# Kernel tuning notes

Hardware: AMD Instinct MI355X
Metric: run time of the kernel (lower is better)

## Reference

```python
import jax, jax.numpy as jnp
import numpy as np

B, H, W, C = 2, 128, 128, 192
HEADS = 6
HD = C // HEADS
WS = 16
OWIN = int(WS * 0.5) + WS          # 24
PAD = (OWIN - WS) // 2             # 4
NQ = WS * WS
NK = OWIN * OWIN
EPS = 1e-6
HID = ((int(C * 2.667) + 7) // 8) * 8  # 512


def _rel_pos_index():
    cq = np.stack(np.meshgrid(np.arange(WS), np.arange(WS), indexing='ij')).reshape(2, -1)
    ck = np.stack(np.meshgrid(np.arange(OWIN), np.arange(OWIN), indexing='ij')).reshape(2, -1)
    rel = (ck[:, None, :] - cq[:, :, None]).transpose(1, 2, 0).astype(np.int64)  # (nq, nk, 2)
    rel[:, :, 0] += WS - 1
    rel[:, :, 1] += WS - 1
    rel[:, :, 0] *= WS + OWIN - 1
    return rel.sum(-1)  # (nq, nk)

RPI = jnp.asarray(_rel_pos_index())


def setup_inputs() -> dict:
    key = jax.random.key(0)
    ks = jax.random.split(key, 16)
    def w(k, shape, s=0.02):
        return jax.random.normal(k, shape, jnp.float32) * s
    return {
        'x': jax.random.normal(ks[0], (B, H * W, C), jnp.float32),
        'qkv_w': w(ks[1], (3 * C, C)), 'qkv_b': jnp.zeros((3 * C,), jnp.float32),
        'proj_w': w(ks[2], (C, C)), 'proj_b': jnp.zeros((C,), jnp.float32),
        'rpb': w(ks[3], ((WS + OWIN - 1) ** 2, HEADS)),
        'n1_w': jnp.ones((C,), jnp.float32), 'n1_b': jnp.zeros((C,), jnp.float32),
        'ls1': jnp.full((C,), 1e-6, jnp.float32),
        'n2_w': jnp.ones((C,), jnp.float32), 'n2_b': jnp.zeros((C,), jnp.float32),
        'ls2': jnp.full((C,), 1e-6, jnp.float32),
        'fcgv_w': w(ks[4], (2 * HID, C)), 'fcgv_b': jnp.zeros((2 * HID,), jnp.float32),
        'dw_w': w(ks[5], (HID, 1, 3, 3)), 'dw_b': jnp.zeros((HID,), jnp.float32),
        'dwd_w': w(ks[6], (HID, 1, 3, 3)), 'dwd_b': jnp.zeros((HID,), jnp.float32),
        'dil_scale': w(ks[7], (1,), 0.1),
        'fco_w': w(ks[8], (C, HID)), 'fco_b': jnp.zeros((C,), jnp.float32),
    }


def _iln(x, wgt, bias):
    # spatially-holistic LN: stats over (L, C); returns normed x and residual scale
    xf = x.astype(jnp.float32)
    mean = xf.mean(axis=(1, 2), keepdims=True)
    var = ((xf - mean) ** 2).mean(axis=(1, 2), keepdims=True)
    std = jnp.sqrt(var + EPS)
    scale = jnp.minimum(std, 2.0)  # std_ema buffer initialized to 1.0 (eval path)
    xn = (xf - mean) / scale
    return (xn * wgt + bias).astype(x.dtype), scale


def _oca(x, qkv_w, qkv_b, proj_w, proj_b, rpb):
    b = x.shape[0]
    nh, nw = H // WS, W // WS
    nwin = b * nh * nw
    qkv = x @ qkv_w.T + qkv_b
    q, k, v = jnp.split(qkv, 3, axis=-1)
    # non-overlapping query windows: (nwin, heads, nq, hd)
    qw = q.reshape(b, nh, WS, nw, WS, C).transpose(0, 1, 3, 2, 4, 5)
    qw = qw.reshape(nwin, NQ, HEADS, HD).transpose(0, 2, 1, 3)
    # overlapping K/V windows via unfold(kernel=OWIN, stride=WS, pad=PAD)
    kv = jnp.concatenate([k, v], axis=-1).reshape(b, H, W, 2 * C).transpose(0, 3, 1, 2)
    kvp = jnp.pad(kv, ((0, 0), (0, 0), (PAD, PAD), (PAD, PAD)))
    ih = (jnp.arange(nh) * WS)[:, None] + jnp.arange(OWIN)[None, :]
    iw = (jnp.arange(nw) * WS)[:, None] + jnp.arange(OWIN)[None, :]
    kvw = kvp[:, :, ih][:, :, :, :, iw]               # (b, 2C, nh, owin, nw, owin)
    kvw = kvw.transpose(0, 2, 4, 3, 5, 1).reshape(nwin, NK, 2 * C)
    kw = kvw[..., :C].reshape(nwin, NK, HEADS, HD).transpose(0, 2, 1, 3)
    vw = kvw[..., C:].reshape(nwin, NK, HEADS, HD).transpose(0, 2, 1, 3)
    bias = rpb[RPI].transpose(2, 0, 1)                # (heads, nq, nk)
    logits = jnp.einsum('whqd,whkd->whqk', qw, kw) * (HD ** -0.5) + bias
    attn = jax.nn.softmax(logits, axis=-1)
    out = jnp.einsum('whqk,whkd->whqd', attn, vw)
    out = out.transpose(0, 2, 1, 3).reshape(nwin, NQ, C) @ proj_w.T + proj_b
    # window reverse -> (b, H*W, C)
    out = out.reshape(b, nh, nw, WS, WS, C).transpose(0, 1, 3, 2, 4, 5).reshape(b, H * W, C)
    return out


def _dw(x, wgt, bias, dil):
    y = jax.lax.conv_general_dilated(x, wgt, (1, 1), [(dil, dil), (dil, dil)],
                                     rhs_dilation=(dil, dil), feature_group_count=HID)
    return y + bias[None, :, None, None]


def _ffn(x, fcgv_w, fcgv_b, dw_w, dw_b, dwd_w, dwd_b, dil_scale, fco_w, fco_b):
    gv = x @ fcgv_w.T + fcgv_b
    g, val = jnp.split(gv, 2, axis=-1)
    h = jax.nn.silu(g) * val
    h = h.transpose(0, 2, 1).reshape(-1, HID, H, W)
    h = _dw(h, dw_w, dw_b, 1)
    h = h + dil_scale[0] * _dw(h, dwd_w, dwd_b, 2)
    h = h.reshape(-1, HID, H * W).transpose(0, 2, 1)
    return h @ fco_w.T + fco_b


def reference(x, qkv_w, qkv_b, proj_w, proj_b, rpb, n1_w, n1_b, ls1, n2_w, n2_b, ls2,
              fcgv_w, fcgv_b, dw_w, dw_b, dwd_w, dwd_b, dil_scale, fco_w, fco_b):
    xn, std1 = _iln(x, n1_w, n1_b)
    x = x + std1 * (ls1 * _oca(xn, qkv_w, qkv_b, proj_w, proj_b, rpb))
    xn2, std2 = _iln(x, n2_w, n2_b)
    x = x + std2 * (ls2 * _ffn(xn2, fcgv_w, fcgv_b, dw_w, dw_b, dwd_w, dwd_b, dil_scale, fco_w, fco_b))
    return x
```

## Files before the change

kernel.cpp:

```cpp
#include <hip/hip_runtime.h>

#define DI __device__ __forceinline__

typedef __attribute__((ext_vector_type(8))) short bh8;
typedef __attribute__((ext_vector_type(4))) float fx4;
typedef __attribute__((ext_vector_type(16))) float fx16;

DI short f2bf(float f) {
  unsigned u = __builtin_bit_cast(unsigned, f);
  u += 0x7FFFu + ((u >> 16) & 1u);
  return (short)(u >> 16);
}
DI float bf2f(short s) {
  unsigned u = ((unsigned)(unsigned short)s) << 16;
  return __builtin_bit_cast(float, u);
}
DI fx4 mfma16(bh8 a, bh8 b, fx4 c) {
  return __builtin_amdgcn_mfma_f32_16x16x32_bf16(a, b, c, 0, 0, 0);
}
DI fx16 mfma32(bh8 a, bh8 b, fx16 c) {
  return __builtin_amdgcn_mfma_f32_32x32x16_bf16(a, b, c, 0, 0, 0);
}
DI fx4 fzero() { fx4 z = {0.f, 0.f, 0.f, 0.f}; return z; }

// ... 28 lines not shown
__global__ __launch_bounds__(256) void iln_partial(const float* __restrict__ x,
                                                   float* __restrict__ part) {
  const int blk = blockIdx.x, tid = threadIdx.x;
  const fx4* p = (const fx4*)(x + (size_t)blk * 12288);
  float s = 0.f, s2 = 0.f;
#pragma unroll
  for (int i = 0; i < 12; i++) {
    fx4 v = p[i * 256 + tid];
    s  += v[0] + v[1] + v[2] + v[3];
    s2 += v[0] * v[0] + v[1] * v[1] + v[2] * v[2] + v[3] * v[3];
  }
  __shared__ float sm[512];
  sm[tid] = s; sm[256 + tid] = s2;
  __syncthreads();
  for (int st = 128; st > 0; st >>= 1) {
    if (tid < st) { sm[tid] += sm[tid + st]; sm[256 + tid] += sm[256 + tid + st]; }
    __syncthreads();
  }
  if (tid == 0) { part[blk * 2] = sm[0]; part[blk * 2 + 1] = sm[256]; }
}

__global__ __launch_bounds__(256) void iln_final(const float* __restrict__ part,
                                                 const float* __restrict__ w,
                                                 const float* __restrict__ bias,
                                                 float* __restrict__ aff,
                                                 float* __restrict__ st) {
  const int b = blockIdx.x, tid = threadIdx.x;
  __shared__ float sm[512];
  sm[tid]       = part[(b * 256 + tid) * 2];
  sm[256 + tid] = part[(b * 256 + tid) * 2 + 1];
  __syncthreads();
  for (int s = 128; s > 0; s >>= 1) {
    if (tid < s) { sm[tid] += sm[tid + s]; sm[256 + tid] += sm[256 + tid + s]; }
    __syncthreads();
  }
  const float invn = 1.f / 3145728.f;
  float mean = sm[0] * invn;
  float var  = sm[256] * invn - mean * mean;
  float scale = fminf(sqrtf(var + 1e-6f), 2.f);
  if (tid < 192) {
    float a = w[tid] / scale;
    aff[(b * 192 + tid) * 2]     = a;
    aff[(b * 192 + tid) * 2 + 1] = bias[tid] - mean * a;
  }
  if (tid == 0) { st[b * 2] = mean; st[b * 2 + 1] = scale; }
}

__global__ __launch_bounds__(256) void cvt_w(const float* __restrict__ qkv_w,
                                             const float* __restrict__ proj_w,
                                             const float* __restrict__ fcgv_w,
                                             const float* __restrict__ fco_w,
                                             short* __restrict__ wbuf) {
  int t = blockIdx.x * 256 + threadIdx.x;
  int off = t * 8;
  const float* src;
  if (off < 110592)       src = qkv_w + off;
  else if (off < 147456)  src = proj_w + (off - 110592);
  else if (off < 344064)  src = fcgv_w + (off - 147456);
  else                    src = fco_w + (off - 344064);
  *(bh8*)(wbuf + off) = pack8(src);
}

__global__ __launch_bounds__(256) void cvt_aff(const float* __restrict__ src,
                                               const float* __restrict__ aff,
                                               short* __restrict__ dst) {
  int t = blockIdx.x * 256 + threadIdx.x;
  int row = t / 24;
  int c0 = (t - row * 24) * 8;
  const float* affp = aff + (row >> 14) * 384 + c0 * 2;
  *(bh8*)(dst + (size_t)t * 8) = pack8_aff(src + (size_t)row * 192 + c0, affp);
}

__global__ __launch_bounds__(256) void bias_gen(const float* __restrict__ rpb,
                                                float* __restrict__ btf) {
  int t = blockIdx.x * 256 + threadIdx.x;
  int lane = t & 63;
  int u = t >> 6;
  int qi = u & 1; int u2 = u >> 1;
  int ki = u2 & 1; u2 >>= 1;
  int kc = u2 % 9; u2 = u2 / 9;
  int w = u2 & 3, head = u2 >> 2;
  int c = lane & 31, hi = lane >> 5;
  int q = w * 64 + qi * 32 + c;
  int qterm = (q >> 4) * 39 + (q & 15);
  (void)ki; (void)kc;
  float o[16];
#pragma unroll
  for (int r = 0; r < 16; r++) {
    int k = (u & 0x3c) ? 0 : 0;
    (void)k;
    int kk = ((u >> 2) % 9) * 64 + ((u >> 1) & 1) * 32 + (r & 3) + 8 * (r >> 2) + 4 * hi;
    int ky = (kk * 2731) >> 16;
    int kx = kk - ky * 24;
    int idx = ky * 39 + kx + 600 - qterm;
    o[r] = rpb[idx * 6 + head] * 1.4426950408889634f;
  }
  fx4* dst = (fx4*)btf;
#pragma unroll
  for (int j = 0; j < 4; j++) {
    fx4 v = {o[4 * j], o[4 * j + 1], o[4 * j + 2], o[4 * j + 3]};
    dst[((size_t)u * 4 + j) * 64 + lane] = v;
  }
}

__global__ __launch_bounds__(256) void gemm_qkv(const short* __restrict__ xn,
                                                const short* __restrict__ wq,
                                                const float* __restrict__ wb,
                                                short* __restrict__ qb,
                                                short* __restrict__ kb,
                                                short* __restrict__ vb) {
  __shared__ short As[128 * 40];
  __shared__ short Bs[96 * 40];
  const int m0 = blockIdx.x * 128, by = blockIdx.y, n0 = by * 96;
  const int tid = threadIdx.x, wid = tid >> 6, lane = tid & 63;
  const int g = lane >> 4, h = lane & 15;
  const int wm = wid >> 1, wn = wid & 1;
  fx4 acc[4][3];
#pragma unroll
  for (int i = 0; i < 4; i++)
#pragma unroll
    for (int j = 0; j < 3; j++) acc[i][j] = fzero();

  for (int kt = 0; kt < 6; kt++) {
    const int k0 = kt * 32;
#pragma unroll
    for (int i = 0; i < 2; i++) {
      int ch = tid + i * 256;
      int row = ch >> 2, sl = ch & 3;
      *(bh8*)&As[row * 40 + sl * 8] = *(const bh8*)(xn + (size_t)(m0 + row) * 192 + k0 + sl * 8);
    }
    {
      int row = tid >> 2, sl = tid & 3;
      *(bh8*)&Bs[row * 40 + sl * 8] = *(const bh8*)(wq + (size_t)(n0 + row) * 192 + k0 + sl * 8);
      int ch = tid + 256;
      if (ch < 384) {
        row = ch >> 2; sl = ch & 3;
        *(bh8*)&Bs[row * 40 + sl * 8] = *(const bh8*)(wq + (size_t)(n0 + row) * 192 + k0 + sl * 8);
      }
    }
    __syncthreads();
    bh8 af[4];
#pragma unroll
    for (int mi = 0; mi < 4; mi++)
      af[mi] = *(bh8*)&As[(wm * 64 + mi * 16 + h) * 40 + g * 8];
#pragma unroll
    for (int ni = 0; ni < 3; ni++) {
      bh8 bf = *(bh8*)&Bs[(wn * 48 + ni * 16 + h) * 40 + g * 8];
#pragma unroll
      for (int mi = 0; mi < 4; mi++) acc[mi][ni] = mfma16(af[mi], bf, acc[mi][ni]);
    }
    __syncthreads();
  }
  const int seg = by >> 1;
  short* dst = (seg == 0) ? qb : (seg == 1 ? kb : vb);
  const float sc = (seg == 1) ? 0.25503486f : 1.0f;
  const int colbase = (by & 1) * 96;
#pragma unroll
  for (int mi = 0; mi < 4; mi++)
#pragma unroll
    for (int ni = 0; ni < 3; ni++)
#pragma unroll
      for (int r = 0; r < 4; r++) {
        int row = m0 + wm * 64 + mi * 16 + g * 4 + r;
        int col = colbase + wn * 48 + ni * 16 + h;
        dst[(size_t)row * 192 + col] = f2bf((acc[mi][ni][r] + wb[seg * 192 + col]) * sc);
      }
}

__global__ __launch_bounds__(256, 3) void attn_kernel(const short* __restrict__ qb,
                                                      const short* __restrict__ kb,
                                                      const short* __restrict__ vb,
                                                      const float* __restrict__ btf,
                                                      short* __restrict__ ao) {
  __shared__ short K_lds[2][64 * 40];
  __shared__ short Vt_lds[2][32 * 72];
  __shared__ float l_lds[256];
  const int tid = threadIdx.x;
  const int win = blockIdx.x, head = blockIdx.y;
  const int b = win >> 6, wy = (win >> 3) & 7, wx = win & 7;
  const int w = tid >> 6, lane = tid & 63, c = lane & 31, hi = lane >> 5;

  bh8 qf[2][2];
#pragma unroll
  for (int qi = 0; qi < 2; qi++) {
    int ql = w * 64 + qi * 32 + c;
    size_t gl = (size_t)(b * 16384 + (wy * 16 + (ql >> 4)) * 128 + wx * 16 + (ql & 15));
#pragma unroll
    for (int ds = 0; ds < 2; ds++)
      qf[qi][ds] = *(const bh8*)(qb + gl * 192 + head * 32 + ds * 16 + hi * 8);
  }
  float l_run[2] = {0.f, 0.f};
  fx16 out[2];
#pragma unroll
  for (int r = 0; r < 16; r++) { out[0][r] = 0.f; out[1][r] = 0.f; }

  const fx4* btf4 = (const fx4*)btf;
  const int hw9 = (head * 4 + w) * 9;

  const int kl_a = tid >> 2, part_a = tid & 3;
  const int kl_b = tid & 63, hg_b = tid >> 6;

  auto load_kv = [&](int kc, bh8& kr, bh8& vr) {
    int key = kc * 64 + kl_a;
    int ky = key / 24, kx = key - ky * 24;
    int py = wy * 16 - 4 + ky, px = wx * 16 - 4 + kx;
    bh8 kv = {};
    if ((unsigned)py < 128u && (unsigned)px < 128u)
      kv = *(const bh8*)(kb + ((size_t)(b * 16384 + py * 128 + px)) * 192 + head * 32 + part_a * 8);
    kr = kv;
    int key2 = kc * 64 + kl_b;
    int ky2 = key2 / 24, kx2 = key2 - ky2 * 24;
    int py2 = wy * 16 - 4 + ky2, px2 = wx * 16 - 4 + kx2;
    bh8 vv = {};
    if ((unsigned)py2 < 128u && (unsigned)px2 < 128u)
      vv = *(const bh8*)(vb + ((size_t)(b * 16384 + py2 * 128 + px2)) * 192 + head * 32 + hg_b * 8);
    vr = vv;
  };

  {
    bh8 k0r, v0r;
    load_kv(0, k0r, v0r);
    *(bh8*)&K_lds[0][kl_a * 40 + part_a * 8] = k0r;
#pragma unroll
    for (int j = 0; j < 8; j++) Vt_lds[0][(hg_b * 8 + j) * 72 + kl_b] = v0r[j];
  }
  int cur = 0;

  for (int kc = 0; kc < 9; kc++) {
    bh8 kn, vn;
    if (kc < 8) load_kv(kc + 1, kn, vn);
    __syncthreads();

    const fx4* base_kc = btf4 + (size_t)(hw9 + kc) * 1024 + lane;
#pragma unroll
    for (int ki = 0; ki < 2; ki++) {
      fx16 st[2];
#pragma unroll
      for (int qi = 0; qi < 2; qi++) {
        const fx4* bp = base_kc + (ki * 2 + qi) * 256;
        fx4 b0 = bp[0], b1 = bp[64], b2 = bp[128], b3 = bp[192];
#pragma unroll
        for (int m = 0; m < 4; m++) {
          st[qi][m]      = b0[m];
          st[qi][4 + m]  = b1[m];
          st[qi][8 + m]  = b2[m];
          st[qi][12 + m] = b3[m];
        }
      }
#pragma unroll
      for (int ds = 0; ds < 2; ds++) {
        bh8 kf = *(bh8*)&K_lds[cur][(ki * 32 + c) * 40 + ds * 16 + hi * 8];
        st[0] = mfma32(kf, qf[0][ds], st[0]);
        st[1] = mfma32(kf, qf[1][ds], st[1]);
      }
#pragma unroll
      for (int qi = 0; qi < 2; qi++) {
        float s = 0.f;
#pragma unroll
        for (int r = 0; r < 16; r++) {
          float p = fexp2(st[qi][r]);
          st[qi][r] = p;
          s += p;
        }
        l_run[qi] += s;
      }
      int dwq[2][2][4];
#pragma unroll
      for (int qi = 0; qi < 2; qi++)
#pragma unroll
        for (int k1 = 0; k1 < 2; k1++)
#pragma unroll
          for (int p01 = 0; p01 < 2; p01++) {
            int rA = 2 * p01 + 8 * k1;
            int A, Bv;
            asm("v_cvt_pk_bf16_f32 %0, %1, %2" : "=v"(A)  : "v"(st[qi][rA]),     "v"(st[qi][rA + 1]));
            asm("v_cvt_pk_bf16_f32 %0, %1, %2" : "=v"(Bv) : "v"(st[qi][rA + 4]), "v"(st[qi][rA + 5]));
#if __has_builtin(__builtin_amdgcn_permlane32_swap)
            auto pr = __builtin_amdgcn_permlane32_swap((unsigned)A, (unsigned)Bv, false, false);
            dwq[qi][k1][p01]     = (int)pr[0];
            dwq[qi][k1][p01 + 2] = (int)pr[1];
#else
            int Ax = __shfl_xor(A, 32);
            int Bx = __shfl_xor(Bv, 32);
            dwq[qi][k1][p01]     = hi ? Bx : A;
            dwq[qi][k1][p01 + 2] = hi ? Bv : Ax;
#endif
          }
#pragma unroll
      for (int k1 = 0; k1 < 2; k1++) {
        bh8 bv2 = *(bh8*)&Vt_lds[cur][c * 72 + (ki * 2 + k1) * 16 + hi * 8];
#pragma unroll
        for (int qi = 0; qi < 2; qi++) {
          int4 t4 = {dwq[qi][k1][0], dwq[qi][k1][1], dwq[qi][k1][2], dwq[qi][k1][3]};
          out[qi] = mfma32(__builtin_bit_cast(bh8, t4), bv2, out[qi]);
        }
      }
    }
    if (kc < 8) {
      *(bh8*)&K_lds[cur ^ 1][kl_a * 40 + part_a * 8] = kn;
#pragma unroll
      for (int j = 0; j < 8; j++) Vt_lds[cur ^ 1][(hg_b * 8 + j) * 72 + kl_b] = vn[j];
    }
    cur ^= 1;
  }
#pragma unroll
  for (int qi = 0; qi < 2; qi++) {
    float lp = l_run[qi] + __shfl_xor(l_run[qi], 32);
    l_lds[w * 64 + qi * 32 + c] = 1.f / lp;
  }
  __syncthreads();
#pragma unroll
  for (int qi = 0; qi < 2; qi++)
#pragma unroll
    for (int r = 0; r < 16; r++) {
      int row = (r & 3) + 8 * (r >> 2) + 4 * hi;
      float val = out[qi][r] * l_lds[w * 64 + qi * 32 + row];
      int ql = w * 64 + qi * 32 + row;
      ao[((size_t)(win * 256 + ql)) * 192 + head * 32 + c] = f2bf(val);
    }
}

__global__ __launch_bounds__(256) void gemm_proj(const short* __restrict__ ao,
                                                 const short* __restrict__ wp,
                                                 const float* __restrict__ wb,
                                                 const float* __restrict__ x,
                                                 const float* __restrict__ ls1,
                                                 const float* __restrict__ st,
                                                 float* __restrict__ x1,
                                                 float* __restrict__ part2) {
  __shared__ short As[128 * 40];
  __shared__ short Bs[96 * 40];
  const int m0 = blockIdx.x * 128, by = blockIdx.y, n0 = by * 96;
  const int tid = threadIdx.x, wid = tid >> 6, lane = tid & 63;
  const int g = lane >> 4, h = lane & 15;
  const int wm = wid >> 1, wn = wid & 1;
  fx4 acc[4][3];
#pragma unroll
  for (int i = 0; i < 4; i++)
#pragma unroll
    for (int j = 0; j < 3; j++) acc[i][j] = fzero();

  for (int kt = 0; kt < 6; kt++) {
    const int k0 = kt * 32;
#pragma unroll
    for (int i = 0; i < 2; i++) {
      int ch = tid + i * 256;
      int row = ch >> 2, sl = ch & 3;
      *(bh8*)&As[row * 40 + sl * 8] = *(const bh8*)(ao + (size_t)(m0 + row) * 192 + k0 + sl * 8);
    }
    {
      int row = tid >> 2, sl = tid & 3;
      *(bh8*)&Bs[row * 40 + sl * 8] = *(const bh8*)(wp + (size_t)(n0 + row) * 192 + k0 + sl * 8);
      int ch = tid + 256;
      if (ch < 384) {
        row = ch >> 2; sl = ch & 3;
        *(bh8*)&Bs[row * 40 + sl * 8] = *(const bh8*)(wp + (size_t)(n0 + row) * 192 + k0 + sl * 8);
      }
    }
    __syncthreads();
    bh8 af[4];
#pragma unroll
    for (int mi = 0; mi < 4; mi++)
      af[mi] = *(bh8*)&As[(wm * 64 + mi * 16 + h) * 40 + g * 8];
#pragma unroll
    for (int ni = 0; ni < 3; ni++) {
      bh8 bf = *(bh8*)&Bs[(wn * 48 + ni * 16 + h) * 40 + g * 8];
#pragma unroll
      for (int mi = 0; mi < 4; mi++) acc[mi][ni] = mfma16(af[mi], bf, acc[mi][ni]);
    }
    __syncthreads();
  }
  float ps = 0.f, ps2 = 0.f;
#pragma unroll
  for (int mi = 0; mi < 4; mi++)
#pragma unroll
    for (int ni = 0; ni < 3; ni++)
#pragma unroll
      for (int r = 0; r < 4; r++) {
        int grow = m0 + wm * 64 + mi * 16 + g * 4 + r;
        int win = grow >> 8, q = grow & 255;
        int bb = win >> 6, wy = (win >> 3) & 7, wxx = win & 7;
        int l = (wy * 16 + (q >> 4)) * 128 + wxx * 16 + (q & 15);
        int col = n0 + wn * 48 + ni * 16 + h;
        size_t di = ((size_t)(bb * 16384 + l)) * 192 + col;
        float s1 = st[bb * 2 + 1];
        float val = x[di] + s1 * ls1[col] * (acc[mi][ni][r] + wb[col]);
        x1[di] = val;
        ps += val;
        ps2 += val * val;
      }
  float* red = (float*)As;
  red[tid] = ps; red[256 + tid] = ps2;
  __syncthreads();
  for (int s = 128; s > 0; s >>= 1) {
    if (tid < s) { red[tid] += red[tid + s]; red[256 + tid] += red[256 + tid + s]; }
    __syncthreads();
  }
  if (tid == 0) {
    int pi = blockIdx.x * 2 + by;
    part2[pi * 2] = red[0];
    part2[pi * 2 + 1] = red[256];
  }
}

__global__ __launch_bounds__(256) void gemm_fcgv(const short* __restrict__ x1n,
                                                 const short* __restrict__ wg,
                                                 const float* __restrict__ wb,
                                                 short* __restrict__ hp) {
  __shared__ short smem[128 * 40 + 128 * 40];
  short* As = smem;
  short* Bs = smem + 128 * 40;
  const int m0 = blockIdx.x * 128, n0 = blockIdx.y * 64;
  const int b = m0 >> 14, l0 = m0 & 16383;
  const int tid = threadIdx.x, wid = tid >> 6, lane = tid & 63;
  const int g = lane >> 4, h = lane & 15;
  const int wm = wid >> 1, wn = wid & 1;
  fx4 accg[4][2], accv[4][2];
#pragma unroll
  for (int i = 0; i < 4; i++)
#pragma unroll
    for (int j = 0; j < 2; j++) { accg[i][j] = fzero(); accv[i][j] = fzero(); }

  for (int kt = 0; kt < 6; kt++) {
    const int k0 = kt * 32;
#pragma unroll
    for (int i = 0; i < 2; i++) {
      int ch = tid + i * 256;
      int row = ch >> 2, sl = ch & 3;
      *(bh8*)&As[row * 40 + sl * 8] = *(const bh8*)(x1n + (size_t)(m0 + row) * 192 + k0 + sl * 8);
    }
#pragma unroll
    for (int i = 0; i < 2; i++) {
      int ch = tid + i * 256;
      int row = ch >> 2, sl = ch & 3;
      int wrow = (row < 64) ? (n0 + row) : (512 + n0 + row - 64);
      *(bh8*)&Bs[row * 40 + sl * 8] = *(const bh8*)(wg + (size_t)wrow * 192 + k0 + sl * 8);
    }
    __syncthreads();
    bh8 af[4];
#pragma unroll
    for (int mi = 0; mi < 4; mi++)
      af[mi] = *(bh8*)&As[(wm * 64 + mi * 16 + h) * 40 + g * 8];
#pragma unroll
    for (int ni = 0; ni < 2; ni++) {
      bh8 bg = *(bh8*)&Bs[(wn * 32 + ni * 16 + h) * 40 + g * 8];
      bh8 bv = *(bh8*)&Bs[(64 + wn * 32 + ni * 16 + h) * 40 + g * 8];
#pragma unroll
      for (int mi = 0; mi < 4; mi++) {
        accg[mi][ni] = mfma16(af[mi], bg, accg[mi][ni]);
        accv[mi][ni] = mfma16(af[mi], bv, accv[mi][ni]);
      }
    }
    __syncthreads();
  }
  short hs[4][2][4];
#pragma unroll
  for (int mi = 0; mi < 4; mi++)
#pragma unroll
    for (int ni = 0; ni < 2; ni++)
#pragma unroll
      for (int r = 0; r < 4; r++) {
        int colg = n0 + wn * 32 + ni * 16 + h;
        float gv = accg[mi][ni][r] + wb[colg];
        float vv = accv[mi][ni][r] + wb[512 + colg];
        hs[mi][ni][r] = f2bf(gv / (1.f + __expf(-gv)) * vv);
      }
  short* T = smem;
#pragma unroll
  for (int mi = 0; mi < 4; mi++)
#pragma unroll
    for (int ni = 0; ni < 2; ni++)
#pragma unroll
      for (int r = 0; r < 4; r++) {
        int cc = wn * 32 + ni * 16 + h;
        int rl = wm * 64 + mi * 16 + g * 4 + r;
        T[cc * 136 + rl] = hs[mi][ni][r];
      }
  __syncthreads();
#pragma unroll
  for (int i = 0; i < 4; i++) {
    int ch = tid + i * 256;
    int cc = ch >> 4, lg = ch & 15;
    bh8 v = *(bh8*)&T[cc * 136 + lg * 8];
    *(bh8*)(hp + (((size_t)(b * 512 + n0 + cc)) << 14) + l0 + lg * 8) = v;
  }
}

__global__ __launch_bounds__(256, 2) void dw_fused(const short* __restrict__ in,
                                                   const float* __restrict__ w1,
                                                   const float* __restrict__ b1,
                                                   const float* __restrict__ w2,
                                                   const float* __restrict__ b2,
                                                   const float* __restrict__ dsc,
                                                   short* __restrict__ outp) {
  __shared__ short P[136 * 128];
  __shared__ short D[136 * 128];
  const int p = blockIdx.x, c = p & 511;
  const int tid = threadIdx.x;
#pragma unroll
  for (int i = 0; i < 8; i++) {
    int gs = i * 256 + tid;
    int yy = gs >> 4, sl = gs & 15;
    bh8 v = *(const bh8*)(in + ((size_t)p << 14) + gs * 8);
    *(bh8*)&P[yy * 136 + sl * 8] = v;
  }
  float k1[9], k2[9];
#pragma unroll
  for (int j = 0; j < 9; j++) { k1[j] = w1[c * 9 + j]; k2[j] = w2[c * 9 + j]; }
  const float bias1 = b1[c], bias2 = b2[c], ds = dsc[0];
  const int y = tid >> 1, hf = tid & 1;
  __syncthreads();

#pragma unroll
  for (int g = 0; g < 8; g++) {
    const int x0 = hf * 64 + g * 8;
    float acc[8];
#pragma unroll
    for (int i = 0; i < 8; i++) acc[i] = bias1;
#pragma unroll
    for (int ky = 0; ky < 3; ky++) {
// ... 19 lines not shown
  __syncthreads();

#pragma unroll
  for (int g = 0; g < 8; g++) {
    const int x0 = hf * 64 + g * 8;
    float acc[8], center[8];
#pragma unroll
    for (int i = 0; i < 8; i++) acc[i] = bias2;
#pragma unroll
    for (int ky = 0; ky < 3; ky++) {
      int yy = y + (ky - 1) * 2;
      if ((unsigned)yy < 128u) {
        const short* row = &D[yy * 136];
        float f[12];
        bh8 v = *(const bh8*)&row[x0];
#pragma unroll
        for (int j = 0; j < 8; j++) f[j + 2] = bf2f(v[j]);
        if (x0 == 0) { f[0] = 0.f; f[1] = 0.f; }
        else {
          unsigned lp = *(const unsigned*)&row[x0 - 2];
          f[0] = __builtin_bit_cast(float, lp << 16);
          f[1] = __builtin_bit_cast(float, lp & 0xffff0000u);
        }
        if (x0 == 120) { f[10] = 0.f; f[11] = 0.f; }
        else {
          unsigned rp = *(const unsigned*)&row[x0 + 8];
          f[10] = __builtin_bit_cast(float, rp << 16);
          f[11] = __builtin_bit_cast(float, rp & 0xffff0000u);
        }
        float w0 = k2[ky * 3], wA = k2[ky * 3 + 1], wB = k2[ky * 3 + 2];
#pragma unroll
        for (int i = 0; i < 8; i++) acc[i] += f[i] * w0 + f[i + 2] * wA + f[i + 4] * wB;
        if (ky == 1) {
#pragma unroll
          for (int i = 0; i < 8; i++) center[i] = f[i + 2];
        }
      }
    }
    bh8 pk;
#pragma unroll
    for (int i = 0; i < 8; i++) pk[i] = f2bf(center[i] + ds * acc[i]);
    *(bh8*)(outp + ((size_t)p << 14) + y * 128 + x0) = pk;
  }
}

__global__ __launch_bounds__(256) void gemm_fco(const short* __restrict__ h2,
                                                const short* __restrict__ wo,
                                                const float* __restrict__ wb,
                                                const float* __restrict__ x1,
                                                const float* __restrict__ ls2,
                                                const float* __restrict__ st,
                                                float* __restrict__ out) {
  __shared__ short As[128 * 40];
  __shared__ short Bs[96 * 40];
  const int m0 = blockIdx.x * 128, by = blockIdx.y, n0 = by * 96;
  const int b = m0 >> 14, l0 = m0 & 16383;
  const int tid = threadIdx.x, wid = tid >> 6, lane = tid & 63;
  const int g = lane >> 4, h = lane & 15;
  const int wm = wid >> 1, wn = wid & 1;
  const int cp = tid & 15, lg = tid >> 4;
  fx4 acc[4][3];
#pragma unroll
  for (int i = 0; i < 4; i++)
#pragma unroll
    for (int j = 0; j < 3; j++) acc[i][j] = fzero();

  for (int kt = 0; kt < 16; kt++) {
    const int k0 = kt * 32;
    {
      const short* basep = h2 + (((size_t)(b * 512 + k0 + 2 * cp)) << 14) + l0 + lg * 8;
      bh8 v0 = *(const bh8*)basep;
      bh8 v1 = *(const bh8*)(basep + 16384);
#pragma unroll
      for (int j = 0; j < 8; j++) {
        unsigned pkv = (unsigned)(unsigned short)v0[j] | (((unsigned)(unsigned short)v1[j]) << 16);
        *(unsigned*)&As[(lg * 8 + j) * 40 + 2 * cp] = pkv;
      }
    }
    {
      int row = tid >> 2, sl = tid & 3;
      *(bh8*)&Bs[row * 40 + sl * 8] = *(const bh8*)(wo + (size_t)(n0 + row) * 512 + k0 + sl * 8);
      int ch = tid + 256;
      if (ch < 384) {
        row = ch >> 2; sl = ch & 3;
        *(bh8*)&Bs[row * 40 + sl * 8] = *(const bh8*)(wo + (size_t)(n0 + row) * 512 + k0 + sl * 8);
      }
    }
    __syncthreads();
    bh8 af[4];
#pragma unroll
    for (int mi = 0; mi < 4; mi++)
      af[mi] = *(bh8*)&As[(wm * 64 + mi * 16 + h) * 40 + g * 8];
#pragma unroll
    for (int ni = 0; ni < 3; ni++) {
      bh8 bf = *(bh8*)&Bs[(wn * 48 + ni * 16 + h) * 40 + g * 8];
#pragma unroll
      for (int mi = 0; mi < 4; mi++) acc[mi][ni] = mfma16(af[mi], bf, acc[mi][ni]);
    }
    __syncthreads();
  }
  float s2 = st[b * 2 + 1];
#pragma unroll
  for (int mi = 0; mi < 4; mi++)
#pragma unroll
    for (int ni = 0; ni < 3; ni++)
#pragma unroll
      for (int r = 0; r < 4; r++) {
        int row = m0 + wm * 64 + mi * 16 + g * 4 + r;
        int col = n0 + wn * 48 + ni * 16 + h;
        size_t di = (size_t)row * 192 + col;
        out[di] = x1[di] + s2 * ls2[col] * (acc[mi][ni][r] + wb[col]);
      }
}

extern "C" void kernel_launch(void* const* d_in, const int* in_sizes, int n_in,
                              void* d_out, int out_size, void* d_ws, size_t ws_size,
                              hipStream_t stream) {
  const float* x      = (const float*)d_in[0];
  const float* qkv_w  = (const float*)d_in[1];
  const float* qkv_b  = (const float*)d_in[2];
  const float* proj_w = (const float*)d_in[3];
  const float* proj_b = (const float*)d_in[4];
  const float* rpb    = (const float*)d_in[5];
  const float* n1_w   = (const float*)d_in[6];
  const float* n1_b   = (const float*)d_in[7];
  const float* ls1    = (const float*)d_in[8];
  const float* n2_w   = (const float*)d_in[9];
  const float* n2_b   = (const float*)d_in[10];
  const float* ls2    = (const float*)d_in[11];
  const float* fcgv_w = (const float*)d_in[12];
  const float* fcgv_b = (const float*)d_in[13];
  const float* dw_w   = (const float*)d_in[14];
  const float* dw_b   = (const float*)d_in[15];
  const float* dwd_w  = (const float*)d_in[16];
  const float* dwd_b  = (const float*)d_in[17];
  const float* dil    = (const float*)d_in[18];
  const float* fco_w  = (const float*)d_in[19];
  const float* fco_b  = (const float*)d_in[20];
  float* out = (float*)d_out;
  char* ws = (char*)d_ws;

  short* wbuf = (short*)(ws + 0);
  short* wq = wbuf;
  short* wp = wbuf + 110592;
  short* wg = wbuf + 147456;
  short* wo = wbuf + 344064;
  float* part  = (float*)(ws + 884736);
  float* aff1  = (float*)(ws + 888832);
  float* aff2  = (float*)(ws + 890368);
  float* st1   = (float*)(ws + 891904);
  float* st2   = (float*)(ws + 891968);
  float* part2 = (float*)(ws + 892032);
  short* xn  = (short*)(ws + 1048576);
  float* btf = (float*)(ws + 13631488);
  short* qb  = (short*)(ws + 17301504);
  short* kb  = (short*)(ws + 29884416);
  short* vb  = (short*)(ws + 42467328);
  short* ao  = (short*)(ws + 55050240);
  float* x1  = (float*)(ws + 1048576);
  short* x1n = (short*)(ws + 26214400);
  short* hp  = (short*)(ws + 42467328);

  cvt_w<<<216, 256, 0, stream>>>(qkv_w, proj_w, fcgv_w, fco_w, wbuf);
  iln_partial<<<512, 256, 0, stream>>>(x, part);
  iln_final<<<2, 256, 0, stream>>>(part, n1_w, n1_b, aff1, st1);
  cvt_aff<<<3072, 256, 0, stream>>>(x, aff1, xn);
  bias_gen<<<216, 256, 0, stream>>>(rpb, btf);
  gemm_qkv<<<dim3(256, 6), 256, 0, stream>>>(xn, wq, qkv_b, qb, kb, vb);
  attn_kernel<<<dim3(128, 6), 256, 0, stream>>>(qb, kb, vb, btf, ao);
  gemm_proj<<<dim3(256, 2), 256, 0, stream>>>(ao, wp, proj_b, x, ls1, st1, x1, part2);
  iln_final<<<2, 256, 0, stream>>>(part2, n2_w, n2_b, aff2, st2);
  cvt_aff<<<3072, 256, 0, stream>>>(x1, aff2, x1n);
  gemm_fcgv<<<dim3(256, 8), 256, 0, stream>>>(x1n, wg, fcgv_b, hp);
  dw_fused<<<1024, 256, 0, stream>>>(hp, dw_w, dw_b, dwd_w, dwd_b, dil, hp);
  gemm_fco<<<dim3(256, 2), 256, 0, stream>>>(hp, wo, fco_b, x1, ls2, st2, out);
}
```

Before: 189.7 us.

## Split attention query rows across two blocks per window-head for more parallelism

The attention kernel now launches two blocks per (window, head), each handling 128 queries with one 32-row query tile per wave instead of two. This doubles the grid from 768 to 1536 blocks and lowers per-thread register use, raising the occupancy hint to 6 blocks per CU, so more waves are available to hide latency on a chip with many CUs. The cost is that each K/V chunk is loaded from global memory and staged into LDS twice, once per half-block. The row-sum is also rewritten as a tree reduction, and a dead statement in bias_gen is removed.

```diff
diff --git a/kernel.cpp b/kernel.cpp
--- a/kernel.cpp
+++ b/kernel.cpp
@@ -139,8 +139,6 @@
   float o[16];
 #pragma unroll
   for (int r = 0; r < 16; r++) {
-    int k = (u & 0x3c) ? 0 : 0;
-    (void)k;
     int kk = ((u >> 2) % 9) * 64 + ((u >> 1) & 1) * 32 + (r & 3) + 8 * (r >> 2) + 4 * hi;
     int ky = (kk * 2731) >> 16;
     int kx = kk - ky * 24;
@@ -219,35 +217,36 @@
       }
 }
 
-__global__ __launch_bounds__(256, 3) void attn_kernel(const short* __restrict__ qb,
+__global__ __launch_bounds__(256, 6) void attn_kernel(const short* __restrict__ qb,
                                                       const short* __restrict__ kb,
                                                       const short* __restrict__ vb,
                                                       const float* __restrict__ btf,
                                                       short* __restrict__ ao) {
   __shared__ short K_lds[2][64 * 40];
   __shared__ short Vt_lds[2][32 * 72];
-  __shared__ float l_lds[256];
+  __shared__ float l_lds[128];
   const int tid = threadIdx.x;
-  const int win = blockIdx.x, head = blockIdx.y;
+  const int win = blockIdx.x >> 1, qh = blockIdx.x & 1, head = blockIdx.y;
   const int b = win >> 6, wy = (win >> 3) & 7, wx = win & 7;
   const int w = tid >> 6, lane = tid & 63, c = lane & 31, hi = lane >> 5;
-
-  bh8 qf[2][2];
-#pragma unroll
-  for (int qi = 0; qi < 2; qi++) {
-    int ql = w * 64 + qi * 32 + c;
+  const int qblk = qh * 4 + w;
+  const int worig = qblk >> 1, qi = qblk & 1;
+
+  bh8 qf[2];
+  {
+    int ql = qblk * 32 + c;
     size_t gl = (size_t)(b * 16384 + (wy * 16 + (ql >> 4)) * 128 + wx * 16 + (ql & 15));
 #pragma unroll
     for (int ds = 0; ds < 2; ds++)
-      qf[qi][ds] = *(const bh8*)(qb + gl * 192 + head * 32 + ds * 16 + hi * 8);
-  }
-  float l_run[2] = {0.f, 0.f};
-  fx16 out[2];
-#pragma unroll
-  for (int r = 0; r < 16; r++) { out[0][r] = 0.f; out[1][r] = 0.f; }
+      qf[ds] = *(const bh8*)(qb + gl * 192 + head * 32 + ds * 16 + hi * 8);
+  }
+  float l_run = 0.f;
+  fx16 out;
+#pragma unroll
+  for (int r = 0; r < 16; r++) out[r] = 0.f;
 
   const fx4* btf4 = (const fx4*)btf;
-  const int hw9 = (head * 4 + w) * 9;
+  const int hw9 = (head * 4 + worig) * 9;
 
   const int kl_a = tid >> 2, part_a = tid & 3;
   const int kl_b = tid & 63, hg_b = tid >> 6;
@@ -283,69 +282,65 @@
     if (kc < 8) load_kv(kc + 1, kn, vn);
     __syncthreads();
 
-    const fx4* base_kc = btf4 + (size_t)(hw9 + kc) * 1024 + lane;
+    const fx4* base_kc = btf4 + (size_t)(hw9 + kc) * 1024 + qi * 256 + lane;
 #pragma unroll
     for (int ki = 0; ki < 2; ki++) {
-      fx16 st[2];
-#pragma unroll
-      for (int qi = 0; qi < 2; qi++) {
-        const fx4* bp = base_kc + (ki * 2 + qi) * 256;
+      fx16 st;
+      {
+        const fx4* bp = base_kc + ki * 512;
         fx4 b0 = bp[0], b1 = bp[64], b2 = bp[128], b3 = bp[192];
 #pragma unroll
         for (int m = 0; m < 4; m++) {
-          st[qi][m]      = b0[m];
-          st[qi][4 + m]  = b1[m];
-          st[qi][8 + m]  = b2[m];
-          st[qi][12 + m] = b3[m];
+          st[m]      = b0[m];
+          st[4 + m]  = b1[m];
+          st[8 + m]  = b2[m];
+          st[12 + m] = b3[m];
         }
       }
 #pragma unroll
       for (int ds = 0; ds < 2; ds++) {
         bh8 kf = *(bh8*)&K_lds[cur][(ki * 32 + c) * 40 + ds * 16 + hi * 8];
-        st[0] = mfma32(kf, qf[0][ds], st[0]);
-        st[1] = mfma32(kf, qf[1][ds], st[1]);
-      }
-#pragma unroll
-      for (int qi = 0; qi < 2; qi++) {
-        float s = 0.f;
+        st = mfma32(kf, qf[ds], st);
+      }
+      {
+        float s[16];
 #pragma unroll
         for (int r = 0; r < 16; r++) {
-          float p = fexp2(st[qi][r]);
-          st[qi][r] = p;
-          s += p;
+          float p = fexp2(st[r]);
+          st[r] = p;
+          s[r] = p;
         }
-        l_run[qi] += s;
-      }
-      int dwq[2][2][4];
-#pragma unroll
-      for (int qi = 0; qi < 2; qi++)
-#pragma unroll
-        for (int k1 = 0; k1 < 2; k1++)
-#pragma unroll
-          for (int p01 = 0; p01 < 2; p01++) {
-            int rA = 2 * p01 + 8 * k1;
-            int A, Bv;
-            asm("v_cvt_pk_bf16_f32 %0, %1, %2" : "=v"(A)  : "v"(st[qi][rA]),     "v"(st[qi][rA + 1]));
-            asm("v_cvt_pk_bf16_f32 %0, %1, %2" : "=v"(Bv) : "v"(st[qi][rA + 4]), "v"(st[qi][rA + 5]));
+#pragma unroll
+        for (int d = 1; d < 16; d <<= 1)
+#pragma unroll
+          for (int r = 0; r < 16; r += 2 * d) s[r] += s[r + d];
+        l_run += s[0];
+      }
+      int dwq[2][4];
+#pragma unroll
+      for (int k1 = 0; k1 < 2; k1++)
+#pragma unroll
+        for (int p01 = 0; p01 < 2; p01++) {
+          int rA = 2 * p01 + 8 * k1;
+          int A, Bv;
+          asm("v_cvt_pk_bf16_f32 %0, %1, %2" : "=v"(A)  : "v"(st[rA]),     "v"(st[rA + 1]));
+          asm("v_cvt_pk_bf16_f32 %0, %1, %2" : "=v"(Bv) : "v"(st[rA + 4]), "v"(st[rA + 5]));
 #if __has_builtin(__builtin_amdgcn_permlane32_swap)
-            auto pr = __builtin_amdgcn_permlane32_swap((unsigned)A, (unsigned)Bv, false, false);
-            dwq[qi][k1][p01]     = (int)pr[0];
-            dwq[qi][k1][p01 + 2] = (int)pr[1];
+          auto pr = __builtin_amdgcn_permlane32_swap((unsigned)A, (unsigned)Bv, false, false);
+          dwq[k1][p01]     = (int)pr[0];
+          dwq[k1][p01 + 2] = (int)pr[1];
 #else
-            int Ax = __shfl_xor(A, 32);
-            int Bx = __shfl_xor(Bv, 32);
-            dwq[qi][k1][p01]     = hi ? Bx : A;
-            dwq[qi][k1][p01 + 2] = hi ? Bv : Ax;
+          int Ax = __shfl_xor(A, 32);
+          int Bx = __shfl_xor(Bv, 32);
+          dwq[k1][p01]     = hi ? Bx : A;
+          dwq[k1][p01 + 2] = hi ? Bv : Ax;
 #endif
-          }
+        }
 #pragma unroll
       for (int k1 = 0; k1 < 2; k1++) {
         bh8 bv2 = *(bh8*)&Vt_lds[cur][c * 72 + (ki * 2 + k1) * 16 + hi * 8];
-#pragma unroll
-        for (int qi = 0; qi < 2; qi++) {
-          int4 t4 = {dwq[qi][k1][0], dwq[qi][k1][1], dwq[qi][k1][2], dwq[qi][k1][3]};
-          out[qi] = mfma32(__builtin_bit_cast(bh8, t4), bv2, out[qi]);
-        }
+        int4 t4 = {dwq[k1][0], dwq[k1][1], dwq[k1][2], dwq[k1][3]};
+        out = mfma32(__builtin_bit_cast(bh8, t4), bv2, out);
       }
     }
     if (kc < 8) {
@@ -355,21 +350,18 @@
     }
     cur ^= 1;
   }
-#pragma unroll
-  for (int qi = 0; qi < 2; qi++) {
-    float lp = l_run[qi] + __shfl_xor(l_run[qi], 32);
-    l_lds[w * 64 + qi * 32 + c] = 1.f / lp;
+  {
+    float lp = l_run + __shfl_xor(l_run, 32);
+    l_lds[w * 32 + c] = 1.f / lp;
   }
   __syncthreads();
 #pragma unroll
-  for (int qi = 0; qi < 2; qi++)
-#pragma unroll
-    for (int r = 0; r < 16; r++) {
-      int row = (r & 3) + 8 * (r >> 2) + 4 * hi;
-      float val = out[qi][r] * l_lds[w * 64 + qi * 32 + row];
-      int ql = w * 64 + qi * 32 + row;
-      ao[((size_t)(win * 256 + ql)) * 192 + head * 32 + c] = f2bf(val);
-    }
+  for (int r = 0; r < 16; r++) {
+    int row = (r & 3) + 8 * (r >> 2) + 4 * hi;
+    float val = out[r] * l_lds[w * 32 + row];
+    int ql = qblk * 32 + row;
+    ao[((size_t)(win * 256 + ql)) * 192 + head * 32 + c] = f2bf(val);
+  }
 }
 
 __global__ __launch_bounds__(256) void gemm_proj(const short* __restrict__ ao,
@@ -758,7 +750,7 @@
   cvt_aff<<<3072, 256, 0, stream>>>(x, aff1, xn);
   bias_gen<<<216, 256, 0, stream>>>(rpb, btf);
   gemm_qkv<<<dim3(256, 6), 256, 0, stream>>>(xn, wq, qkv_b, qb, kb, vb);
-  attn_kernel<<<dim3(128, 6), 256, 0, stream>>>(qb, kb, vb, btf, ao);
+  attn_kernel<<<dim3(256, 6), 256, 0, stream>>>(qb, kb, vb, btf, ao);
   gemm_proj<<<dim3(256, 2), 256, 0, stream>>>(ao, wp, proj_b, x, ls1, st1, x1, part2);
   iln_final<<<2, 256, 0, stream>>>(part2, n2_w, n2_b, aff2, st2);
   cvt_aff<<<3072, 256, 0, stream>>>(x1, aff2, x1n);
```

Result: slower. 246.5 us (+30.0%).

## Pre-swizzle weights and activations into MFMA fragment order; drop LDS staging

Applied to the files above, without the earlier changes.

Weight conversion and the normalized-activation conversion now write bf16 data directly in the per-lane MFMA fragment layout. This lets the qkv, proj, fcgv and fco GEMMs load operands straight from global memory into registers, removing the LDS staging and its barriers. The attention kernel also drops K/V double buffering in favor of a single buffer with a sync before each load. Fewer barriers and less LDS use should improve occupancy, but the attention kernel loses its load/compute overlap and the GEMMs now rely on cache for operand reuse across waves.

```diff
diff --git a/kernel.cpp b/kernel.cpp
--- a/kernel.cpp
+++ b/kernel.cpp
@@ -104,13 +104,42 @@
                                              const float* __restrict__ fco_w,
                                              short* __restrict__ wbuf) {
   int t = blockIdx.x * 256 + threadIdx.x;
-  int off = t * 8;
+  int blk = t >> 6, lane = t & 63;
+  int g = lane >> 4, h = lane & 15;
   const float* src;
-  if (off < 110592)       src = qkv_w + off;
-  else if (off < 147456)  src = proj_w + (off - 110592);
-  else if (off < 344064)  src = fcgv_w + (off - 147456);
-  else                    src = fco_w + (off - 344064);
-  *(bh8*)(wbuf + off) = pack8(src);
+  if (blk < 216) {
+    int b2 = blk;
+    int ni = b2 % 3; b2 /= 3;
+    int wn = b2 & 1; b2 >>= 1;
+    int kt = b2 % 6; b2 /= 6;
+    int nt = b2;
+    src = qkv_w + (size_t)(nt * 96 + wn * 48 + ni * 16 + h) * 192 + kt * 32 + g * 8;
+  } else if (blk < 288) {
+    int b2 = blk - 216;
+    int ni = b2 % 3; b2 /= 3;
+    int wn = b2 & 1; b2 >>= 1;
+    int kt = b2 % 6; b2 /= 6;
+    int nt = b2;
+    src = proj_w + (size_t)(nt * 96 + wn * 48 + ni * 16 + h) * 192 + kt * 32 + g * 8;
+  } else if (blk < 672) {
+    int b2 = blk - 288;
+    int gv = b2 & 1; b2 >>= 1;
+    int ni = b2 & 1; b2 >>= 1;
+    int wn = b2 & 1; b2 >>= 1;
+    int kt = b2 % 6; b2 /= 6;
+    int nt = b2;
+    int r = wn * 32 + ni * 16 + h;
+    int row = gv ? (512 + nt * 64 + r) : (nt * 64 + r);
+    src = fcgv_w + (size_t)row * 192 + kt * 32 + g * 8;
+  } else {
+    int b2 = blk - 672;
+    int ni = b2 % 3; b2 /= 3;
+    int wn = b2 & 1; b2 >>= 1;
+    int kt = b2 & 15; b2 >>= 4;
+    int nt = b2;
+    src = fco_w + (size_t)(nt * 96 + wn * 48 + ni * 16 + h) * 512 + kt * 32 + g * 8;
+  }
+  *(bh8*)(wbuf + (size_t)blk * 512 + lane * 8) = pack8(src);
 }
 
 __global__ __launch_bounds__(256) void cvt_aff(const float* __restrict__ src,
@@ -120,7 +149,11 @@
   int row = t / 24;
   int c0 = (t - row * 24) * 8;
   const float* affp = aff + (row >> 14) * 384 + c0 * 2;
-  *(bh8*)(dst + (size_t)t * 8) = pack8_aff(src + (size_t)row * 192 + c0, affp);
+  int mt = row >> 7, wm = (row >> 6) & 1, mi = (row >> 4) & 3, h = row & 15;
+  int kt = c0 >> 5, g = (c0 >> 3) & 3;
+  int blk = ((mt * 2 + wm) * 4 + mi) * 6 + kt;
+  int lane = g * 16 + h;
+  *(bh8*)(dst + (size_t)blk * 512 + lane * 8) = pack8_aff(src + (size_t)row * 192 + c0, affp);
 }
 
 __global__ __launch_bounds__(256) void bias_gen(const float* __restrict__ rpb,
@@ -139,8 +172,6 @@
   float o[16];
 #pragma unroll
   for (int r = 0; r < 16; r++) {
-    int k = (u & 0x3c) ? 0 : 0;
-    (void)k;
     int kk = ((u >> 2) % 9) * 64 + ((u >> 1) & 1) * 32 + (r & 3) + 8 * (r >> 2) + 4 * hi;
     int ky = (kk * 2731) >> 16;
     int kx = kk - ky * 24;
@@ -161,9 +192,8 @@
                                                 short* __restrict__ qb,
                                                 short* __restrict__ kb,
                                                 short* __restrict__ vb) {
-  __shared__ short As[128 * 40];
-  __shared__ short Bs[96 * 40];
-  const int m0 = blockIdx.x * 128, by = blockIdx.y, n0 = by * 96;
+  const int mt = blockIdx.x, by = blockIdx.y;
+  const int m0 = mt * 128;
   const int tid = threadIdx.x, wid = tid >> 6, lane = tid & 63;
   const int g = lane >> 4, h = lane & 15;
   const int wm = wid >> 1, wn = wid & 1;
@@ -173,35 +203,19 @@
 #pragma unroll
     for (int j = 0; j < 3; j++) acc[i][j] = fzero();
 
+#pragma unroll
   for (int kt = 0; kt < 6; kt++) {
-    const int k0 = kt * 32;
-#pragma unroll
-    for (int i = 0; i < 2; i++) {
-      int ch = tid + i * 256;
-      int row = ch >> 2, sl = ch & 3;
-      *(bh8*)&As[row * 40 + sl * 8] = *(const bh8*)(xn + (size_t)(m0 + row) * 192 + k0 + sl * 8);
-    }
-    {
-      int row = tid >> 2, sl = tid & 3;
-      *(bh8*)&Bs[row * 40 + sl * 8] = *(const bh8*)(wq + (size_t)(n0 + row) * 192 + k0 + sl * 8);
-      int ch = tid + 256;
-      if (ch < 384) {
-        row = ch >> 2; sl = ch & 3;
-        *(bh8*)&Bs[row * 40 + sl * 8] = *(const bh8*)(wq + (size_t)(n0 + row) * 192 + k0 + sl * 8);
-      }
-    }
-    __syncthreads();
-    bh8 af[4];
+    bh8 af[4], bf[3];
 #pragma unroll
     for (int mi = 0; mi < 4; mi++)
-      af[mi] = *(bh8*)&As[(wm * 64 + mi * 16 + h) * 40 + g * 8];
-#pragma unroll
-    for (int ni = 0; ni < 3; ni++) {
-      bh8 bf = *(bh8*)&Bs[(wn * 48 + ni * 16 + h) * 40 + g * 8];
-#pragma unroll
-      for (int mi = 0; mi < 4; mi++) acc[mi][ni] = mfma16(af[mi], bf, acc[mi][ni]);
-    }
-    __syncthreads();
+      af[mi] = *(const bh8*)(xn + (size_t)((((mt * 2 + wm) * 4 + mi) * 6 + kt)) * 512 + lane * 8);
+#pragma unroll
+    for (int ni = 0; ni < 3; ni++)
+      bf[ni] = *(const bh8*)(wq + (size_t)(((by * 6 + kt) * 2 + wn) * 3 + ni) * 512 + lane * 8);
+#pragma unroll
+    for (int ni = 0; ni < 3; ni++)
+#pragma unroll
+      for (int mi = 0; mi < 4; mi++) acc[mi][ni] = mfma16(af[mi], bf[ni], acc[mi][ni]);
   }
   const int seg = by >> 1;
   short* dst = (seg == 0) ? qb : (seg == 1 ? kb : vb);
@@ -224,8 +238,8 @@
                                                       const short* __restrict__ vb,
                                                       const float* __restrict__ btf,
                                                       short* __restrict__ ao) {
-  __shared__ short K_lds[2][64 * 40];
-  __shared__ short Vt_lds[2][32 * 72];
+  __shared__ short K_lds[64 * 40];
+  __shared__ short Vt_lds[32 * 72];
   __shared__ float l_lds[256];
   const int tid = threadIdx.x;
   const int win = blockIdx.x, head = blockIdx.y;
@@ -252,35 +266,26 @@
   const int kl_a = tid >> 2, part_a = tid & 3;
   const int kl_b = tid & 63, hg_b = tid >> 6;
 
-  auto load_kv = [&](int kc, bh8& kr, bh8& vr) {
-    int key = kc * 64 + kl_a;
-    int ky = key / 24, kx = key - ky * 24;
-    int py = wy * 16 - 4 + ky, px = wx * 16 - 4 + kx;
-    bh8 kv = {};
-    if ((unsigned)py < 128u && (unsigned)px < 128u)
-      kv = *(const bh8*)(kb + ((size_t)(b * 16384 + py * 128 + px)) * 192 + head * 32 + part_a * 8);
-    kr = kv;
-    int key2 = kc * 64 + kl_b;
-    int ky2 = key2 / 24, kx2 = key2 - ky2 * 24;
-    int py2 = wy * 16 - 4 + ky2, px2 = wx * 16 - 4 + kx2;
-    bh8 vv = {};
-    if ((unsigned)py2 < 128u && (unsigned)px2 < 128u)
-      vv = *(const bh8*)(vb + ((size_t)(b * 16384 + py2 * 128 + px2)) * 192 + head * 32 + hg_b * 8);
-    vr = vv;
-  };
-
-  {
-    bh8 k0r, v0r;
-    load_kv(0, k0r, v0r);
-    *(bh8*)&K_lds[0][kl_a * 40 + part_a * 8] = k0r;
-#pragma unroll
-    for (int j = 0; j < 8; j++) Vt_lds[0][(hg_b * 8 + j) * 72 + kl_b] = v0r[j];
-  }
-  int cur = 0;
-
   for (int kc = 0; kc < 9; kc++) {
-    bh8 kn, vn;
-    if (kc < 8) load_kv(kc + 1, kn, vn);
+    __syncthreads();
+    {
+      int key = kc * 64 + kl_a;
+      int ky = key / 24, kx = key - ky * 24;
+      int py = wy * 16 - 4 + ky, px = wx * 16 - 4 + kx;
+      bh8 kv = {};
+      if ((unsigned)py < 128u && (unsigned)px < 128u)
+        kv = *(const bh8*)(kb + ((size_t)(b * 16384 + py * 128 + px)) * 192 + head * 32 + part_a * 8);
+      *(bh8*)&K_lds[kl_a * 40 + part_a * 8] = kv;
+
+      int key2 = kc * 64 + kl_b;
+      int ky2 = key2 / 24, kx2 = key2 - ky2 * 24;
+      int py2 = wy * 16 - 4 + ky2, px2 = wx * 16 - 4 + kx2;
+      bh8 vv = {};
+      if ((unsigned)py2 < 128u && (unsigned)px2 < 128u)
+        vv = *(const bh8*)(vb + ((size_t)(b * 16384 + py2 * 128 + px2)) * 192 + head * 32 + hg_b * 8);
+#pragma unroll
+      for (int j = 0; j < 8; j++) Vt_lds[(hg_b * 8 + j) * 72 + kl_b] = vv[j];
+    }
     __syncthreads();
 
     const fx4* base_kc = btf4 + (size_t)(hw9 + kc) * 1024 + lane;
@@ -301,7 +306,7 @@
       }
 #pragma unroll
       for (int ds = 0; ds < 2; ds++) {
-        bh8 kf = *(bh8*)&K_lds[cur][(ki * 32 + c) * 40 + ds * 16 + hi * 8];
+        bh8 kf = *(bh8*)&K_lds[(ki * 32 + c) * 40 + ds * 16 + hi * 8];
         st[0] = mfma32(kf, qf[0][ds], st[0]);
         st[1] = mfma32(kf, qf[1][ds], st[1]);
       }
@@ -340,7 +345,7 @@
           }
 #pragma unroll
       for (int k1 = 0; k1 < 2; k1++) {
-        bh8 bv2 = *(bh8*)&Vt_lds[cur][c * 72 + (ki * 2 + k1) * 16 + hi * 8];
+        bh8 bv2 = *(bh8*)&Vt_lds[c * 72 + (ki * 2 + k1) * 16 + hi * 8];
 #pragma unroll
         for (int qi = 0; qi < 2; qi++) {
           int4 t4 = {dwq[qi][k1][0], dwq[qi][k1][1], dwq[qi][k1][2], dwq[qi][k1][3]};
@@ -348,12 +353,6 @@
         }
       }
     }
-    if (kc < 8) {
-      *(bh8*)&K_lds[cur ^ 1][kl_a * 40 + part_a * 8] = kn;
-#pragma unroll
-      for (int j = 0; j < 8; j++) Vt_lds[cur ^ 1][(hg_b * 8 + j) * 72 + kl_b] = vn[j];
-    }
-    cur ^= 1;
   }
 #pragma unroll
   for (int qi = 0; qi < 2; qi++) {
@@ -380,9 +379,8 @@
                                                  const float* __restrict__ st,
                                                  float* __restrict__ x1,
                                                  float* __restrict__ part2) {
-  __shared__ short As[128 * 40];
-  __shared__ short Bs[96 * 40];
-  const int m0 = blockIdx.x * 128, by = blockIdx.y, n0 = by * 96;
+  __shared__ float red[512];
+  const int m0 = blockIdx.x * 128, by = blockIdx.y;
   const int tid = threadIdx.x, wid = tid >> 6, lane = tid & 63;
   const int g = lane >> 4, h = lane & 15;
   const int wm = wid >> 1, wn = wid & 1;
@@ -392,36 +390,21 @@
 #pragma unroll
     for (int j = 0; j < 3; j++) acc[i][j] = fzero();
 
+#pragma unroll
   for (int kt = 0; kt < 6; kt++) {
-    const int k0 = kt * 32;
-#pragma unroll
-    for (int i = 0; i < 2; i++) {
-      int ch = tid + i * 256;
-      int row = ch >> 2, sl = ch & 3;
-      *(bh8*)&As[row * 40 + sl * 8] = *(const bh8*)(ao + (size_t)(m0 + row) * 192 + k0 + sl * 8);
-    }
-    {
-      int row = tid >> 2, sl = tid & 3;
-      *(bh8*)&Bs[row * 40 + sl * 8] = *(const bh8*)(wp + (size_t)(n0 + row) * 192 + k0 + sl * 8);
-      int ch = tid + 256;
-      if (ch < 384) {
-        row = ch >> 2; sl = ch & 3;
-        *(bh8*)&Bs[row * 40 + sl * 8] = *(const bh8*)(wp + (size_t)(n0 + row) * 192 + k0 + sl * 8);
-      }
-    }
-    __syncthreads();
-    bh8 af[4];
+    bh8 af[4], bf[3];
 #pragma unroll
     for (int mi = 0; mi < 4; mi++)
-      af[mi] = *(bh8*)&As[(wm * 64 + mi * 16 + h) * 40 + g * 8];
-#pragma unroll
-    for (int ni = 0; ni < 3; ni++) {
-      bh8 bf = *(bh8*)&Bs[(wn * 48 + ni * 16 + h) * 40 + g * 8];
-#pragma unroll
-      for (int mi = 0; mi < 4; mi++) acc[mi][ni] = mfma16(af[mi], bf, acc[mi][ni]);
-    }
-    __syncthreads();
-  }
+      af[mi] = *(const bh8*)(ao + (size_t)(m0 + wm * 64 + mi * 16 + h) * 192 + kt * 32 + g * 8);
+#pragma unroll
+    for (int ni = 0; ni < 3; ni++)
+      bf[ni] = *(const bh8*)(wp + (size_t)(((by * 6 + kt) * 2 + wn) * 3 + ni) * 512 + lane * 8);
+#pragma unroll
+    for (int ni = 0; ni < 3; ni++)
+#pragma unroll
+      for (int mi = 0; mi < 4; mi++) acc[mi][ni] = mfma16(af[mi], bf[ni], acc[mi][ni]);
+  }
+  const int n0 = by * 96;
   float ps = 0.f, ps2 = 0.f;
 #pragma unroll
   for (int mi = 0; mi < 4; mi++)
@@ -441,7 +424,6 @@
         ps += val;
         ps2 += val * val;
       }
-  float* red = (float*)As;
   red[tid] = ps; red[256 + tid] = ps2;
   __syncthreads();
   for (int s = 128; s > 0; s >>= 1) {
@@ -459,10 +441,9 @@
                                                  const short* __restrict__ wg,
                                                  const float* __restrict__ wb,
                                                  short* __restrict__ hp) {
-  __shared__ short smem[128 * 40 + 128 * 40];
-  short* As = smem;
-  short* Bs = smem + 128 * 40;
-  const int m0 = blockIdx.x * 128, n0 = blockIdx.y * 64;
+  __shared__ short T[64 * 136];
+  const int mt = blockIdx.x, by = blockIdx.y, n0 = by * 64;
+  const int m0 = mt * 128;
   const int b = m0 >> 14, l0 = m0 & 16383;
   const int tid = threadIdx.x, wid = tid >> 6, lane = tid & 63;
   const int g = lane >> 4, h = lane & 15;
@@ -473,37 +454,25 @@
 #pragma unroll
     for (int j = 0; j < 2; j++) { accg[i][j] = fzero(); accv[i][j] = fzero(); }
 
+#pragma unroll
   for (int kt = 0; kt < 6; kt++) {
-    const int k0 = kt * 32;
-#pragma unroll
-    for (int i = 0; i < 2; i++) {
-      int ch = tid + i * 256;
-      int row = ch >> 2, sl = ch & 3;
-      *(bh8*)&As[row * 40 + sl * 8] = *(const bh8*)(x1n + (size_t)(m0 + row) * 192 + k0 + sl * 8);
+    bh8 af[4], bg[2], bv[2];
+#pragma unroll
+    for (int mi = 0; mi < 4; mi++)
+      af[mi] = *(const bh8*)(x1n + (size_t)((((mt * 2 + wm) * 4 + mi) * 6 + kt)) * 512 + lane * 8);
+#pragma unroll
+    for (int ni = 0; ni < 2; ni++) {
+      size_t base = (size_t)((((by * 6 + kt) * 2 + wn) * 2 + ni) * 2) * 512;
+      bg[ni] = *(const bh8*)(wg + base + lane * 8);
+      bv[ni] = *(const bh8*)(wg + base + 512 + lane * 8);
     }
 #pragma unroll
-    for (int i = 0; i < 2; i++) {
-      int ch = tid + i * 256;
-      int row = ch >> 2, sl = ch & 3;
-      int wrow = (row < 64) ? (n0 + row) : (512 + n0 + row - 64);
-      *(bh8*)&Bs[row * 40 + sl * 8] = *(const bh8*)(wg + (size_t)wrow * 192 + k0 + sl * 8);
-    }
-    __syncthreads();
-    bh8 af[4];
-#pragma unroll
-    for (int mi = 0; mi < 4; mi++)
-      af[mi] = *(bh8*)&As[(wm * 64 + mi * 16 + h) * 40 + g * 8];
-#pragma unroll
-    for (int ni = 0; ni < 2; ni++) {
-      bh8 bg = *(bh8*)&Bs[(wn * 32 + ni * 16 + h) * 40 + g * 8];
-      bh8 bv = *(bh8*)&Bs[(64 + wn * 32 + ni * 16 + h) * 40 + g * 8];
+    for (int ni = 0; ni < 2; ni++)
 #pragma unroll
       for (int mi = 0; mi < 4; mi++) {
-        accg[mi][ni] = mfma16(af[mi], bg, accg[mi][ni]);
-        accv[mi][ni] = mfma16(af[mi], bv, accv[mi][ni]);
-      }
-    }
-    __syncthreads();
+        accg[mi][ni] = mfma16(af[mi], bg[ni], accg[mi][ni]);
+        accv[mi][ni] = mfma16(af[mi], bv[ni], accv[mi][ni]);
+      }
   }
   short hs[4][2][4];
 #pragma unroll
@@ -517,7 +486,6 @@
         float vv = accv[mi][ni][r] + wb[512 + colg];
         hs[mi][ni][r] = f2bf(gv / (1.f + __expf(-gv)) * vv);
       }
-  short* T = smem;
 #pragma unroll
   for (int mi = 0; mi < 4; mi++)
 #pragma unroll
@@ -643,7 +611,6 @@
                                                 const float* __restrict__ st,
                                                 float* __restrict__ out) {
   __shared__ short As[128 * 40];
-  __shared__ short Bs[96 * 40];
   const int m0 = blockIdx.x * 128, by = blockIdx.y, n0 = by * 96;
   const int b = m0 >> 14, l0 = m0 & 16383;
   const int tid = threadIdx.x, wid = tid >> 6, lane = tid & 63;
@@ -668,26 +635,18 @@
         *(unsigned*)&As[(lg * 8 + j) * 40 + 2 * cp] = pkv;
       }
     }
-    {
-      int row = tid >> 2, sl = tid & 3;
-      *(bh8*)&Bs[row * 40 + sl * 8] = *(const bh8*)(wo + (size_t)(n0 + row) * 512 + k0 + sl * 8);
-      int ch = tid + 256;
-      if (ch < 384) {
-        row = ch >> 2; sl = ch & 3;
-        *(bh8*)&Bs[row * 40 + sl * 8] = *(const bh8*)(wo + (size_t)(n0 + row) * 512 + k0 + sl * 8);
-      }
-    }
     __syncthreads();
-    bh8 af[4];
+    bh8 af[4], bf[3];
 #pragma unroll
     for (int mi = 0; mi < 4; mi++)
       af[mi] = *(bh8*)&As[(wm * 64 + mi * 16 + h) * 40 + g * 8];
 #pragma unroll
-    for (int ni = 0; ni < 3; ni++) {
-      bh8 bf = *(bh8*)&Bs[(wn * 48 + ni * 16 + h) * 40 + g * 8];
-#pragma unroll
-      for (int mi = 0; mi < 4; mi++) acc[mi][ni] = mfma16(af[mi], bf, acc[mi][ni]);
-    }
+    for (int ni = 0; ni < 3; ni++)
+      bf[ni] = *(const bh8*)(wo + (size_t)(((by * 16 + kt) * 2 + wn) * 3 + ni) * 512 + lane * 8);
+#pragma unroll
+    for (int ni = 0; ni < 3; ni++)
+#pragma unroll
+      for (int mi = 0; mi < 4; mi++) acc[mi][ni] = mfma16(af[mi], bf[ni], acc[mi][ni]);
     __syncthreads();
   }
   float s2 = st[b * 2 + 1];
```

After: 185.2 us. 1.02x faster.
